# Kernel optimization log

Hardware: AMD Instinct MI355X
Metric: run time of the kernel (lower is better)

Reference implementation:

```python
import jax, jax.numpy as jnp
import numpy as np
from jax import lax

N_STEPS = 96
N_MAT = 4
N_STRIKES = 201
PERIOD = N_STEPS // N_MAT  # 24
BATCH = 8192
T_HORIZON = 2.0
RFR = 0.05
S0 = 100.0
DT = T_HORIZON / N_STEPS
SQRT_DT = DT ** 0.5
DF = float(np.exp(-RFR * DT))  # one-step discount factor


def _drift_nets(p, x):
    # x: [3, B]; three stacked MLPs (sigma_S, b_V, sigma_V), n=net axis -> [3, 1, B]
    W0, b0, W1, b1, W2, b2, W3, b3 = p
    h = jax.nn.relu(jnp.einsum('nof,fb->nob', W0, x) + b0[:, :, None])
    h = jax.nn.relu(jnp.einsum('nof,nfb->nob', W1, h) + b1[:, :, None])
    h = jax.nn.relu(jnp.einsum('nof,nfb->nob', W2, h) + b2[:, :, None])
    return jnp.einsum('nof,nfb->nob', W3, h) + b3[:, :, None]


def _hedge_net(p, x):
    # x: [2, B] -> [N_STRIKES*N_MAT, B]
    W0, b0, W1, b1, W2, b2, W3, b3, W4, b4 = p
    h = jax.nn.relu(W0 @ x + b0[:, None])
    h = jax.nn.relu(W1 @ h + b1[:, None])
    h = jax.nn.relu(W2 @ h + b2[:, None])
    h = jax.nn.relu(W3 @ h + b3[:, None])
    return W4 @ h + b4[:, None]


def _forward(nW0, nb0, nW1, nb1, nW2, nb2, nW3, nb3,
             hW0, hb0, hW1, hb1, hW2, hb2, hW3, hb3, hW4, hb4,
             rho, V0, strikes, noise1, noise2, remat=False):
    dtype = noise1.dtype
    B = noise1.shape[1]
    rho_s = rho[0]
    S = jnp.full((B,), S0, dtype)
    V = jnp.ones((B,), dtype) * V0[0]
    H = jnp.zeros((N_STRIKES, N_MAT, B), dtype)  # hedging accumulator
    prices = jnp.zeros((N_STRIKES, N_MAT), dtype)
    variance = jnp.zeros((N_STRIKES, N_MAT), dtype)
    for m in range(N_MAT):  # one MLP set per maturity period (timegridNet idx)
        nP = (nW0[:, m], nb0[:, m], nW1[:, m], nb1[:, m],
              nW2[:, m], nb2[:, m], nW3[:, m], nb3[:, m])
        hP = (hW0[m], hb0[m], hW1[m], hb1[m], hW2[m], hb2[m],
              hW3[m], hb3[m], hW4[m], hb4[m])

        def step(carry, xs, nP=nP, hP=hP):
            S, V, H = carry
            t_i, n1, n2 = xs
            t = t_i * jnp.ones_like(S)
            X = jnp.stack([t, S, V], 0)  # [3, B]
            raw = _drift_nets(nP, X)
            raw_d = _drift_nets(nP, lax.stop_gradient(X))  # X.detach() path
            vals = raw / (1.0 + jnp.abs(raw_d) * SQRT_DT)
            sig_S, b_V, sig_V = vals[0, 0], vals[1, 0], vals[2, 0]
            b_S = S * RFR / (1.0 + jnp.abs(lax.stop_gradient(S) * RFR) * SQRT_DT)
            dW = SQRT_DT * n2
            dB = rho_s * dW + jnp.sqrt(1.0 - rho_s ** 2) * SQRT_DT * n1
            S_new = S + b_S * DT + sig_S * dB
            V_new = jax.nn.relu(V + b_V * DT + sig_V * dW)  # clamp(.., 0)
            hedge = _hedge_net(hP, jnp.stack([t, lax.stop_gradient(S)], 0))
            hedge = hedge.reshape(N_STRIKES, N_MAT, -1)
            H_new = H + DF * lax.stop_gradient(S) * lax.stop_gradient(sig_S) * hedge * dW
            return (S_new, V_new, H_new), None

        if remat:
            step = jax.checkpoint(step)
        ts = (jnp.arange(PERIOD, dtype=dtype) + m * PERIOD) * DT  # (i-1)*dt
        xs = (ts, noise1[m * PERIOD:(m + 1) * PERIOD], noise2[m * PERIOD:(m + 1) * PERIOD])
        (S, V, H), _ = lax.scan(step, (S, V, H), xs)
        disc = DF ** ((m + 1) * PERIOD)
        payoff = disc * jax.nn.relu(S[None, :] - strikes) - H[:, m]  # [201, B]
        prices = prices.at[:, m].set(jnp.mean(payoff, axis=1))
        variance = variance.at[:, m].set(jnp.var(payoff, axis=1, ddof=1))  # torch unbiased var
    return prices, variance


def setup_inputs() -> dict:
    key = jax.random.key(0)
    ks = jax.random.split(key, 24)
    f32 = jnp.float32

    def w(k, shape, fan_in):
        return (jax.random.normal(k, shape, f32) / np.sqrt(fan_in)).astype(f32)

    def b(k, shape):
        return 0.01 * jax.random.normal(k, shape, f32)

    inp = {}
    inp['nW0'] = w(ks[0], (3, 4, 32, 3), 3)
    inp['nb0'] = b(ks[1], (3, 4, 32))
    inp['nW1'] = w(ks[2], (3, 4, 32, 32), 32)
    inp['nb1'] = b(ks[3], (3, 4, 32))
    inp['nW2'] = w(ks[4], (3, 4, 32, 32), 32)
    inp['nb2'] = b(ks[5], (3, 4, 32))
    inp['nW3'] = w(ks[6], (3, 4, 1, 32), 32)
    inp['nb3'] = b(ks[7], (3, 4, 1))
    inp['hW0'] = w(ks[8], (4, 64, 2), 2)
    inp['hb0'] = b(ks[9], (4, 64))
    inp['hW1'] = w(ks[10], (4, 64, 64), 64)
    inp['hb1'] = b(ks[11], (4, 64))
    inp['hW2'] = w(ks[12], (4, 64, 64), 64)
    inp['hb2'] = b(ks[13], (4, 64))
    inp['hW3'] = w(ks[14], (4, 64, 64), 64)
    inp['hb3'] = b(ks[15], (4, 64))
    inp['hW4'] = w(ks[16], (4, 804, 64), 64)
    inp['hb4'] = b(ks[17], (4, 804))
    inp['rho'] = jnp.array([0.3], f32)
    inp['V0'] = jnp.array([0.04], f32)
    inp['strikes'] = jnp.linspace(50.0, 150.0, N_STRIKES, dtype=f32).reshape(-1, 1)
    inp['noise1'] = jax.random.normal(ks[18], (N_STEPS, BATCH), f32)
    inp['noise2'] = jax.random.normal(ks[19], (N_STEPS, BATCH), f32)
    return inp


def reference(nW0, nb0, nW1, nb1, nW2, nb2, nW3, nb3,
              hW0, hb0, hW1, hb1, hW2, hb2, hW3, hb3, hW4, hb4,
              rho, V0, strikes, noise1, noise2):
    return _forward(nW0, nb0, nW1, nb1, nW2, nb2, nW3, nb3,
                    hW0, hb0, hW1, hb1, hW2, hb2, hW3, hb3, hW4, hb4,
                    rho, V0, strikes, noise1, noise2)
```

## Files before the change

### kernel.cpp

```cpp
#include <hip/hip_runtime.h>
#include <math.h>

#define TPB      128
#define NBLOCKS  512
#define PPB      16
#define BATCHN   8192
#define NMAT     4
#define PERS     24
#define NK       201
#define DSTR     124
#define HSTR     76
#define GSTR     68
#define GSC      (1.0f/4096.0f)
#define GUNSC    4096.0f

typedef _Float16 f16;
typedef _Float16 f16x4 __attribute__((ext_vector_type(4)));
typedef _Float16 f16x8 __attribute__((ext_vector_type(8)));
typedef float    f32x4 __attribute__((ext_vector_type(4)));

template<int N> struct IC { static constexpr int v = N; };

#define LDS_FENCE() asm volatile("s_waitcnt lgkmcnt(0)" ::: "memory")

__device__ __forceinline__ f16x8 relu8(f16x8 v){
#pragma unroll
  for (int i = 0; i < 8; ++i) v[i] = (v[i] > (f16)0.f) ? v[i] : (f16)0.f;
  return v;
}
__device__ __forceinline__ f16x8 cvt88(float4 a, float4 b){
  f16x8 r;
  r[0]=(f16)a.x; r[1]=(f16)a.y; r[2]=(f16)a.z; r[3]=(f16)a.w;
  r[4]=(f16)b.x; r[5]=(f16)b.y; r[6]=(f16)b.z; r[7]=(f16)b.w;
  return r;
}
__device__ __forceinline__ f16x4 cvt4(float4 a){
  f16x4 r; r[0]=(f16)a.x; r[1]=(f16)a.y; r[2]=(f16)a.z; r[3]=(f16)a.w; return r;
}

__global__ __launch_bounds__(TPB, 1)
void sde_kernel(const float* __restrict__ nW0, const float* __restrict__ nb0,
                const float* __restrict__ nW1, const float* __restrict__ nb1,
                const float* __restrict__ nW2, const float* __restrict__ nb2,
                const float* __restrict__ nW3, const float* __restrict__ nb3,
                const float* __restrict__ hW0, const float* __restrict__ hb0,
                const float* __restrict__ hW1, const float* __restrict__ hb1,
                const float* __restrict__ hW2, const float* __restrict__ hb2,
                const float* __restrict__ hW3, const float* __restrict__ hb3,
                const float* __restrict__ hW4, const float* __restrict__ hb4,
                const float* __restrict__ rho, const float* __restrict__ V0,
                const float* __restrict__ strikes,
                const float* __restrict__ noise1, const float* __restrict__ noise2,
                float* __restrict__ part1, float* __restrict__ part2)
{
  __shared__ __align__(16) f16   bbD [PPB*DSTR];
  __shared__ __align__(16) f16   bbH1[PPB*HSTR];
  __shared__ __align__(16) f16   bbH2[PPB*HSTR];
  __shared__ __align__(16) float Gsave[NMAT*PPB*GSTR];
  __shared__ float mbS[2][PPB], mbc[2][PPB];
  __shared__ float CstL[NMAT*PPB];
  __shared__ float SfinL[PPB];
  __shared__ float strikesL[NK];

  const int tid  = threadIdx.x;
  const int wv   = tid >> 6;
  const int lane = tid & 63;
  const int L15  = lane & 15;
  const int G    = lane >> 4;
  const int gpath = blockIdx.x * PPB + L15;

  const float DTf = (float)(2.0/96.0);
  const float SDT = 0.14433756729740643f;
  const float DFf = (float)exp(-0.05 * 2.0 / 96.0);
  const float rho_s = rho[0];
  const float rt1m  = sqrtf(1.f - rho_s*rho_s);

  for (int k = tid; k < NK; k += TPB) strikesL[k] = strikes[k];

  float S = 100.f, Vv = V0[0];
  __syncthreads();

  auto maturity = [&](auto MC){
    constexpr int m = decltype(MC)::v;

    f16x8 aD1[6], aD2[6];  f16x4 bD1r[6], bD2r[6];  f32x4 w3r[6];
    f16x8 w0r[3][4];       float b30=0.f, b31=0.f, b32=0.f;
    f16x8 aH[3][4][2];     f16x4 bHr[3][4];         f16x8 wh0r[2][3];
    float Gacc[16];        float Cacc = 0.f;
    float pn1 = 0.f, pn2 = 0.f;

    if (wv == 0){
#pragma unroll
      for (int t6 = 0; t6 < 6; ++t6){
        const int n  = t6 >> 1;
        const int o  = ((t6 & 1) << 4) + L15;
        const int ob = ((t6 & 1) << 4) + 4*G;
        const float* p1 = nW1 + (size_t)(((n*4+m)*32)+o)*32 + G*8;
        aD1[t6] = cvt88(*(const float4*)p1, *(const float4*)(p1+4));
        const float* p2 = nW2 + (size_t)(((n*4+m)*32)+o)*32 + G*8;
        aD2[t6] = cvt88(*(const float4*)p2, *(const float4*)(p2+4));
        bD1r[t6] = cvt4(*(const float4*)(nb1 + (n*4+m)*32 + ob));
        bD2r[t6] = cvt4(*(const float4*)(nb2 + (n*4+m)*32 + ob));
        w3r[t6]  = *(const f32x4*)(nW3 + (n*4+m)*32 + ob);
      }
      b30 = nb3[m]; b31 = nb3[4+m]; b32 = nb3[8+m];
#pragma unroll
      for (int n = 0; n < 3; ++n){
        f16x8 wt, ws, wvv, bz;
#pragma unroll
        for (int j = 0; j < 8; ++j){
          const int o = G*8 + j;
          const float* p = nW0 + (size_t)(((n*4+m)*32)+o)*3;
          wt[j]=(f16)p[0]; ws[j]=(f16)p[1]; wvv[j]=(f16)p[2];
          bz[j]=(f16)nb0[(n*4+m)*32+o];
        }
        w0r[n][0]=wt; w0r[n][1]=ws; w0r[n][2]=wvv; w0r[n][3]=bz;
      }
      pn1 = noise1[(size_t)(m*PERS)*BATCHN + gpath];
      pn2 = noise2[(size_t)(m*PERS)*BATCHN + gpath];
    } else {
#pragma unroll
      for (int L = 0; L < 3; ++L){
        const float* W = (L==0)?hW1:(L==1)?hW2:hW3;
        const float* B = (L==0)?hb1:(L==1)?hb2:hb3;
#pragma unroll
        for (int mt = 0; mt < 4; ++mt){
#pragma unroll
          for (int kt = 0; kt < 2; ++kt){
            const float* src = W + (size_t)m*4096 + (16*mt + L15)*64 + kt*32 + G*8;
            aH[L][mt][kt] = cvt88(*(const float4*)src, *(const float4*)(src+4));
          }
          bHr[L][mt] = cvt4(*(const float4*)(B + m*64 + mt*16 + 4*G));
        }
      }
#pragma unroll
      for (int kt = 0; kt < 2; ++kt){
        f16x8 wt, ws, bz;
#pragma unroll
        for (int j = 0; j < 8; ++j){
          const int o = kt*32 + G*8 + j;
          wt[j]=(f16)hW0[m*128 + o*2];
          ws[j]=(f16)hW0[m*128 + o*2 + 1];
          bz[j]=(f16)hb0[m*64 + o];
        }
        wh0r[kt][0]=wt; wh0r[kt][1]=ws; wh0r[kt][2]=bz;
      }
#pragma unroll
      for (int j = 0; j < 16; ++j) Gacc[j] = 0.f;
    }

#pragma unroll 1
    for (int i = 0; i <= PERS; ++i){
      if (wv == 0){
        if (i < PERS){
          const int gstep = m*PERS + i;
          const float t = (float)gstep * DTf;
          if (lane < PPB) mbS[i & 1][L15] = S;
          float nn1 = 0.f, nn2 = 0.f;
          if (i+1 < PERS){
            nn1 = noise1[(size_t)(gstep+1)*BATCHN + gpath];
            nn2 = noise2[(size_t)(gstep+1)*BATCHN + gpath];
          }
          const f16 th=(f16)t, Sh=(f16)S, Vh=(f16)Vv;
          f16x8 bfr[3];
#pragma unroll
          for (int n = 0; n < 3; ++n)
            bfr[n] = relu8(w0r[n][0]*th + w0r[n][1]*Sh + w0r[n][2]*Vh + w0r[n][3]);
#pragma unroll
          for (int t6 = 0; t6 < 6; ++t6){
            f32x4 acc = {(float)bD1r[t6][0],(float)bD1r[t6][1],(float)bD1r[t6][2],(float)bD1r[t6][3]};
            acc = __builtin_amdgcn_mfma_f32_16x16x32_f16(aD1[t6], bfr[t6>>1], acc, 0,0,0);
            f16x4 o4;
            o4[0]=(f16)fmaxf(acc[0],0.f); o4[1]=(f16)fmaxf(acc[1],0.f);
            o4[2]=(f16)fmaxf(acc[2],0.f); o4[3]=(f16)fmaxf(acc[3],0.f);
            *(f16x4*)&bbD[L15*DSTR + t6*16 + 4*G] = o4;
          }
          LDS_FENCE();
          f16x8 bl[3];
#pragma unroll
          for (int n = 0; n < 3; ++n)
            bl[n] = *(const f16x8*)&bbD[L15*DSTR + n*32 + G*8];
          f32x4 c2[6];
#pragma unroll
          for (int t6 = 0; t6 < 6; ++t6){
            f32x4 acc = {(float)bD2r[t6][0],(float)bD2r[t6][1],(float)bD2r[t6][2],(float)bD2r[t6][3]};
            c2[t6] = __builtin_amdgcn_mfma_f32_16x16x32_f16(aD2[t6], bl[t6>>1], acc, 0,0,0);
          }
          float pr0=0.f, pr1=0.f, pr2=0.f;
#pragma unroll
          for (int t6 = 0; t6 < 6; ++t6){
            const f32x4 w4 = w3r[t6];
            const float pp = w4[0]*fmaxf(c2[t6][0],0.f)+w4[1]*fmaxf(c2[t6][1],0.f)
                           + w4[2]*fmaxf(c2[t6][2],0.f)+w4[3]*fmaxf(c2[t6][3],0.f);
            if (t6<2) pr0+=pp; else if (t6<4) pr1+=pp; else pr2+=pp;
          }
          pr0 += __shfl_xor(pr0,16); pr0 += __shfl_xor(pr0,32);
          pr1 += __shfl_xor(pr1,16); pr1 += __shfl_xor(pr1,32);
          pr2 += __shfl_xor(pr2,16); pr2 += __shfl_xor(pr2,32);
          const float r0=pr0+b30, r1=pr1+b31, r2=pr2+b32;
          const float sigS = r0/(1.f+fabsf(r0)*SDT);
          const float bV   = r1/(1.f+fabsf(r1)*SDT);
          const float sigV = r2/(1.f+fabsf(r2)*SDT);
          const float sr = S*0.05f;
          const float bS = sr/(1.f+fabsf(sr)*SDT);
          const float dW = SDT*pn2;
          const float dB = rho_s*dW + rt1m*SDT*pn1;
          const float c  = DFf*S*sigS*dW;
          Cacc += c;
          if (lane < PPB) mbc[i & 1][L15] = c;
          S  = S + bS*DTf + sigS*dB;
          Vv = fmaxf(Vv + bV*DTf + sigV*dW, 0.f);
          pn1 = nn1; pn2 = nn2;
        }
      } else {
        if (i >= 1){
          const int s = i - 1;
          const float t = (float)(m*PERS + s) * DTf;
          const float Sj = mbS[s & 1][L15];
          const float c  = mbc[s & 1][L15];
          const f16 th=(f16)t, Sh=(f16)Sj;
          f16x8 bh0 = relu8(wh0r[0][0]*th + wh0r[0][1]*Sh + wh0r[0][2]);
          f16x8 bh1 = relu8(wh0r[1][0]*th + wh0r[1][1]*Sh + wh0r[1][2]);
#pragma unroll
          for (int mt = 0; mt < 4; ++mt){
            f32x4 acc = {(float)bHr[0][mt][0],(float)bHr[0][mt][1],(float)bHr[0][mt][2],(float)bHr[0][mt][3]};
            acc = __builtin_amdgcn_mfma_f32_16x16x32_f16(aH[0][mt][0], bh0, acc, 0,0,0);
            acc = __builtin_amdgcn_mfma_f32_16x16x32_f16(aH[0][mt][1], bh1, acc, 0,0,0);
            f16x4 o4;
            o4[0]=(f16)fmaxf(acc[0],0.f); o4[1]=(f16)fmaxf(acc[1],0.f);
            o4[2]=(f16)fmaxf(acc[2],0.f); o4[3]=(f16)fmaxf(acc[3],0.f);
            *(f16x4*)&bbH1[L15*HSTR + mt*16 + 4*G] = o4;
          }
          LDS_FENCE();
          f16x8 x0 = *(const f16x8*)&bbH1[L15*HSTR +      G*8];
          f16x8 x1 = *(const f16x8*)&bbH1[L15*HSTR + 32 + G*8];
#pragma unroll
          for (int mt = 0; mt < 4; ++mt){
            f32x4 acc = {(float)bHr[1][mt][0],(float)bHr[1][mt][1],(float)bHr[1][mt][2],(float)bHr[1][mt][3]};
            acc = __builtin_amdgcn_mfma_f32_16x16x32_f16(aH[1][mt][0], x0, acc, 0,0,0);
            acc = __builtin_amdgcn_mfma_f32_16x16x32_f16(aH[1][mt][1], x1, acc, 0,0,0);
            f16x4 o4;
            o4[0]=(f16)fmaxf(acc[0],0.f); o4[1]=(f16)fmaxf(acc[1],0.f);
            o4[2]=(f16)fmaxf(acc[2],0.f); o4[3]=(f16)fmaxf(acc[3],0.f);
            *(f16x4*)&bbH2[L15*HSTR + mt*16 + 4*G] = o4;
          }
          LDS_FENCE();
          x0 = *(const f16x8*)&bbH2[L15*HSTR +      G*8];
          x1 = *(const f16x8*)&bbH2[L15*HSTR + 32 + G*8];
#pragma unroll
          for (int mt = 0; mt < 4; ++mt){
            f32x4 acc = {(float)bHr[2][mt][0],(float)bHr[2][mt][1],(float)bHr[2][mt][2],(float)bHr[2][mt][3]};
            acc = __builtin_amdgcn_mfma_f32_16x16x32_f16(aH[2][mt][0], x0, acc, 0,0,0);
            acc = __builtin_amdgcn_mfma_f32_16x16x32_f16(aH[2][mt][1], x1, acc, 0,0,0);
            Gacc[mt*4+0] += c*fmaxf(acc[0],0.f);
            Gacc[mt*4+1] += c*fmaxf(acc[1],0.f);
            Gacc[mt*4+2] += c*fmaxf(acc[2],0.f);
            Gacc[mt*4+3] += c*fmaxf(acc[3],0.f);
          }
        }
      }
      __syncthreads();
    }

    if (wv == 0){
      if (lane < PPB){ SfinL[L15] = S; CstL[m*PPB + L15] = Cacc; }
    } else {
#pragma unroll
      for (int mt = 0; mt < 4; ++mt){
        f32x4 gv = {Gacc[mt*4+0], Gacc[mt*4+1], Gacc[mt*4+2], Gacc[mt*4+3]};
        *(f32x4*)&Gsave[(size_t)(m*PPB + L15)*GSTR + mt*16 + 4*G] = gv;
      }
    }
    __syncthreads();

    {
      const float discm = (float)exp(-0.05*(2.0/96.0)*(double)(PERS*(m+1)));
      const float Sfin = SfinL[L15];
      float Cc[m+1];
      f16x8 Bf[m+1][2];
#pragma unroll
      for (int q = 0; q <= m; ++q){
        Cc[q] = CstL[q*PPB + L15];
#pragma unroll
        for (int kt = 0; kt < 2; ++kt){
          const float* gp = &Gsave[(size_t)(q*PPB + L15)*GSTR + kt*32 + G*8];
          const f32x4 g0 = *(const f32x4*)gp;
          const f32x4 g1 = *(const f32x4*)(gp + 4);
          f16x8 b;
          b[0]=(f16)(g0[0]*GSC); b[1]=(f16)(g0[1]*GSC); b[2]=(f16)(g0[2]*GSC); b[3]=(f16)(g0[3]*GSC);
          b[4]=(f16)(g1[0]*GSC); b[5]=(f16)(g1[1]*GSC); b[6]=(f16)(g1[2]*GSC); b[7]=(f16)(g1[3]*GSC);
          Bf[q][kt] = b;
        }
      }
      for (int mt = wv; mt < 13; mt += 2){
        const int ksr = min(16*mt + L15, 200);
        f32x4 acc = {0.f, 0.f, 0.f, 0.f};
#pragma unroll
        for (int q = 0; q <= m; ++q){
#pragma unroll
          for (int kt = 0; kt < 2; ++kt){
            const float* ap = hW4 + (size_t)(q*804 + ksr*4 + m)*64 + kt*32 + G*8;
            const f16x8 a = cvt88(*(const float4*)ap, *(const float4*)(ap+4));
            acc = __builtin_amdgcn_mfma_f32_16x16x32_f16(a, Bf[q][kt], acc, 0,0,0);
          }
        }
#pragma unroll
        for (int r = 0; r < 4; ++r){
          const int k2  = 16*mt + 4*G + r;
          const int k2c = min(k2, 200);
          float ac = acc[r] * GUNSC;
#pragma unroll
          for (int q = 0; q <= m; ++q)
            ac = fmaf(hb4[q*804 + k2c*4 + m], Cc[q], ac);
          const float pay = discm*fmaxf(Sfin - strikesL[k2c], 0.f) - ac;
          float s1 = pay, s2 = pay*pay;
          s1 += __shfl_xor(s1,1); s1 += __shfl_xor(s1,2);
          s1 += __shfl_xor(s1,4); s1 += __shfl_xor(s1,8);
          s2 += __shfl_xor(s2,1); s2 += __shfl_xor(s2,2);
          s2 += __shfl_xor(s2,4); s2 += __shfl_xor(s2,8);
          if (L15 == 0 && k2 < NK){
            part1[(size_t)(m*NK + k2)*NBLOCKS + blockIdx.x] = s1;
            part2[(size_t)(m*NK + k2)*NBLOCKS + blockIdx.x] = s2;
          }
        }
      }
    }
  };

  maturity(IC<0>{});
  maturity(IC<1>{});
  maturity(IC<2>{});
  maturity(IC<3>{});
}

__global__ __launch_bounds__(256)
void finalize_kernel(const float* __restrict__ part1,
                     const float* __restrict__ part2,
                     float* __restrict__ out)
{
  const int j   = blockIdx.x;
  const int m   = j / NK, k = j % NK;
  const int tid = threadIdx.x;
  double s1 = (double)part1[(size_t)j*NBLOCKS + tid]
            + (double)part1[(size_t)j*NBLOCKS + 256 + tid];
  double s2 = (double)part2[(size_t)j*NBLOCKS + tid]
            + (double)part2[(size_t)j*NBLOCKS + 256 + tid];
#pragma unroll
  for (int d = 32; d > 0; d >>= 1){
    s1 += __shfl_down(s1, d, 64);
    s2 += __shfl_down(s2, d, 64);
  }
  __shared__ double r1[4], r2[4];
  if ((tid & 63) == 0){ r1[tid>>6] = s1; r2[tid>>6] = s2; }
  __syncthreads();
  if (tid == 0){
    const double t1 = r1[0]+r1[1]+r1[2]+r1[3];
    const double t2 = r2[0]+r2[1]+r2[2]+r2[3];
    const double mean = t1 / 8192.0;
    const double var  = (t2 - t1*t1/8192.0) / 8191.0;
    out[k*NMAT + m]            = (float)mean;
    out[NK*NMAT + k*NMAT + m]  = (float)var;
  }
}

extern "C" void kernel_launch(void* const* d_in, const int* in_sizes, int n_in,
                              void* d_out, int out_size, void* d_ws, size_t ws_size,
                              hipStream_t stream)
{
  (void)in_sizes; (void)n_in; (void)out_size; (void)ws_size;
  const float* nW0 = (const float*)d_in[0];
  const float* nb0 = (const float*)d_in[1];
  const float* nW1 = (const float*)d_in[2];
  const float* nb1 = (const float*)d_in[3];
  const float* nW2 = (const float*)d_in[4];
  const float* nb2 = (const float*)d_in[5];
  const float* nW3 = (const float*)d_in[6];
  const float* nb3 = (const float*)d_in[7];
  const float* hW0 = (const float*)d_in[8];
  const float* hb0 = (const float*)d_in[9];
  const float* hW1 = (const float*)d_in[10];
  const float* hb1 = (const float*)d_in[11];
  const float* hW2 = (const float*)d_in[12];
  const float* hb2 = (const float*)d_in[13];
  const float* hW3 = (const float*)d_in[14];
  const float* hb3 = (const float*)d_in[15];
  const float* hW4 = (const float*)d_in[16];
  const float* hb4 = (const float*)d_in[17];
  const float* rho = (const float*)d_in[18];
  const float* V0  = (const float*)d_in[19];
  const float* strikes = (const float*)d_in[20];
  const float* noise1  = (const float*)d_in[21];
  const float* noise2  = (const float*)d_in[22];

  float* part1 = (float*)d_ws;
  float* part2 = part1 + (size_t)NMAT*NK*NBLOCKS;

  sde_kernel<<<NBLOCKS, TPB, 0, stream>>>(nW0, nb0, nW1, nb1, nW2, nb2, nW3, nb3,
                                          hW0, hb0, hW1, hb1, hW2, hb2, hW3, hb3,
                                          hW4, hb4, rho, V0, strikes, noise1, noise2,
                                          part1, part2);

  finalize_kernel<<<NMAT*NK, 256, 0, stream>>>(part1, part2, (float*)d_out);
}
```

Measured before the change: 309.6 us.

## Pipeline SDE producer and hedge consumer across maturities with per-period barriers

Replaces the per-step lockstep between the drift wave and the hedge wave, which used a __syncthreads every time step, with a maturity-level software pipeline. Wave 0 simulates a whole period into double-buffered LDS arrays while wave 1 runs the hedge MLP on the previous period, two steps at a time so MFMA chains interleave. The output projection for each maturity is now done by wave 1 alone, and divisions become reciprocal approximations. This cuts barrier count from about 25 per maturity to one per phase, but the final hW4 projection loses its two-wave split and is serialized on one wave.

```diff
diff --git a/kernel.cpp b/kernel.cpp
--- a/kernel.cpp
+++ b/kernel.cpp
@@ -3,14 +3,13 @@
 
 #define TPB      128
 #define NBLOCKS  512
-#define PPB      16
 #define BATCHN   8192
 #define NMAT     4
 #define PERS     24
 #define NK       201
+#define NPG      512
 #define DSTR     124
 #define HSTR     76
-#define GSTR     68
 #define GSC      (1.0f/4096.0f)
 #define GUNSC    4096.0f
 
@@ -18,8 +17,6 @@
 typedef _Float16 f16x4 __attribute__((ext_vector_type(4)));
 typedef _Float16 f16x8 __attribute__((ext_vector_type(8)));
 typedef float    f32x4 __attribute__((ext_vector_type(4)));
-
-template<int N> struct IC { static constexpr int v = N; };
 
 #define LDS_FENCE() asm volatile("s_waitcnt lgkmcnt(0)" ::: "memory")
 
@@ -36,6 +33,9 @@
 }
 __device__ __forceinline__ f16x4 cvt4(float4 a){
   f16x4 r; r[0]=(f16)a.x; r[1]=(f16)a.y; r[2]=(f16)a.z; r[3]=(f16)a.w; return r;
+}
+__device__ __forceinline__ float sdiv(float x, float s){
+  return x * __builtin_amdgcn_rcpf(fmaf(fabsf(x), s, 1.f));
 }
 
 __global__ __launch_bounds__(TPB, 1)
@@ -53,21 +53,18 @@
                 const float* __restrict__ noise1, const float* __restrict__ noise2,
                 float* __restrict__ part1, float* __restrict__ part2)
 {
-  __shared__ __align__(16) f16   bbD [PPB*DSTR];
-  __shared__ __align__(16) f16   bbH1[PPB*HSTR];
-  __shared__ __align__(16) f16   bbH2[PPB*HSTR];
-  __shared__ __align__(16) float Gsave[NMAT*PPB*GSTR];
-  __shared__ float mbS[2][PPB], mbc[2][PPB];
-  __shared__ float CstL[NMAT*PPB];
-  __shared__ float SfinL[PPB];
-  __shared__ float strikesL[NK];
+  __shared__ __align__(16) f16   bbD[16*DSTR];
+  __shared__ __align__(16) f16   bbH[4][16*HSTR];
+  __shared__ float SP[2][PERS][16], CP[2][PERS][16];
+  __shared__ float SfinAll[NMAT][16], CstAll[NMAT][16];
+  __shared__ float Gsave[NMAT][64][17];
 
   const int tid  = threadIdx.x;
   const int wv   = tid >> 6;
   const int lane = tid & 63;
   const int L15  = lane & 15;
   const int G    = lane >> 4;
-  const int gpath = blockIdx.x * PPB + L15;
+  const int gpath = blockIdx.x * 16 + L15;
 
   const float DTf = (float)(2.0/96.0);
   const float SDT = 0.14433756729740643f;
@@ -75,262 +72,253 @@
   const float rho_s = rho[0];
   const float rt1m  = sqrtf(1.f - rho_s*rho_s);
 
-  for (int k = tid; k < NK; k += TPB) strikesL[k] = strikes[k];
-
   float S = 100.f, Vv = V0[0];
-  __syncthreads();
-
-  auto maturity = [&](auto MC){
-    constexpr int m = decltype(MC)::v;
-
-    f16x8 aD1[6], aD2[6];  f16x4 bD1r[6], bD2r[6];  f32x4 w3r[6];
-    f16x8 w0r[3][4];       float b30=0.f, b31=0.f, b32=0.f;
-    f16x8 aH[3][4][2];     f16x4 bHr[3][4];         f16x8 wh0r[2][3];
-    float Gacc[16];        float Cacc = 0.f;
-    float pn1 = 0.f, pn2 = 0.f;
-
-    if (wv == 0){
+
+  auto produce = [&](int m){
+    f16x8 aD1[6], aD2[6];  f32x4 bD1r[6], bD2r[6], w3r[6];
+    f16x8 w0r[3][4];
+#pragma unroll
+    for (int t6 = 0; t6 < 6; ++t6){
+      const int n  = t6 >> 1;
+      const int o  = ((t6 & 1) << 4) + L15;
+      const int ob = ((t6 & 1) << 4) + 4*G;
+      const float* p1 = nW1 + (size_t)(((n*4+m)*32)+o)*32 + G*8;
+      aD1[t6] = cvt88(*(const float4*)p1, *(const float4*)(p1+4));
+      const float* p2 = nW2 + (size_t)(((n*4+m)*32)+o)*32 + G*8;
+      aD2[t6] = cvt88(*(const float4*)p2, *(const float4*)(p2+4));
+      bD1r[t6] = *(const f32x4*)(nb1 + (n*4+m)*32 + ob);
+      bD2r[t6] = *(const f32x4*)(nb2 + (n*4+m)*32 + ob);
+      w3r[t6]  = *(const f32x4*)(nW3 + (n*4+m)*32 + ob);
+    }
+    const float b30 = nb3[m], b31 = nb3[4+m], b32 = nb3[8+m];
+#pragma unroll
+    for (int n = 0; n < 3; ++n){
+      f16x8 wt, ws, wvv, bz;
+#pragma unroll
+      for (int j = 0; j < 8; ++j){
+        const int o = G*8 + j;
+        const float* p = nW0 + (size_t)(((n*4+m)*32)+o)*3;
+        wt[j]=(f16)p[0]; ws[j]=(f16)p[1]; wvv[j]=(f16)p[2];
+        bz[j]=(f16)nb0[(n*4+m)*32+o];
+      }
+      w0r[n][0]=wt; w0r[n][1]=ws; w0r[n][2]=wvv; w0r[n][3]=bz;
+    }
+    float pn1 = noise1[(size_t)(m*PERS)*BATCHN + gpath];
+    float pn2 = noise2[(size_t)(m*PERS)*BATCHN + gpath];
+    float Cacc = 0.f;
+    const int b = m & 1;
+
+#pragma unroll 1
+    for (int s = 0; s < PERS; ++s){
+      const int gstep = m*PERS + s;
+      const float t = (float)gstep * DTf;
+      float nn1 = 0.f, nn2 = 0.f;
+      if (s+1 < PERS){
+        nn1 = noise1[(size_t)(gstep+1)*BATCHN + gpath];
+        nn2 = noise2[(size_t)(gstep+1)*BATCHN + gpath];
+      }
+      const f16 th=(f16)t, Sh=(f16)S, Vh=(f16)Vv;
+      f16x8 bfr[3];
+#pragma unroll
+      for (int n = 0; n < 3; ++n)
+        bfr[n] = relu8(w0r[n][0]*th + w0r[n][1]*Sh + w0r[n][2]*Vh + w0r[n][3]);
 #pragma unroll
       for (int t6 = 0; t6 < 6; ++t6){
-        const int n  = t6 >> 1;
-        const int o  = ((t6 & 1) << 4) + L15;
-        const int ob = ((t6 & 1) << 4) + 4*G;
-        const float* p1 = nW1 + (size_t)(((n*4+m)*32)+o)*32 + G*8;
-        aD1[t6] = cvt88(*(const float4*)p1, *(const float4*)(p1+4));
-        const float* p2 = nW2 + (size_t)(((n*4+m)*32)+o)*32 + G*8;
-        aD2[t6] = cvt88(*(const float4*)p2, *(const float4*)(p2+4));
-        bD1r[t6] = cvt4(*(const float4*)(nb1 + (n*4+m)*32 + ob));
-        bD2r[t6] = cvt4(*(const float4*)(nb2 + (n*4+m)*32 + ob));
-        w3r[t6]  = *(const f32x4*)(nW3 + (n*4+m)*32 + ob);
-      }
-      b30 = nb3[m]; b31 = nb3[4+m]; b32 = nb3[8+m];
-#pragma unroll
-      for (int n = 0; n < 3; ++n){
-        f16x8 wt, ws, wvv, bz;
+        f32x4 acc = {bD1r[t6][0], bD1r[t6][1], bD1r[t6][2], bD1r[t6][3]};
+        acc = __builtin_amdgcn_mfma_f32_16x16x32_f16(aD1[t6], bfr[t6>>1], acc, 0,0,0);
+        f16x4 o4;
+        o4[0]=(f16)fmaxf(acc[0],0.f); o4[1]=(f16)fmaxf(acc[1],0.f);
+        o4[2]=(f16)fmaxf(acc[2],0.f); o4[3]=(f16)fmaxf(acc[3],0.f);
+        *(f16x4*)&bbD[L15*DSTR + t6*16 + 4*G] = o4;
+      }
+      LDS_FENCE();
+      f16x8 bl[3];
+#pragma unroll
+      for (int n = 0; n < 3; ++n)
+        bl[n] = *(const f16x8*)&bbD[L15*DSTR + n*32 + G*8];
+      f32x4 c2[6];
+#pragma unroll
+      for (int t6 = 0; t6 < 6; ++t6){
+        f32x4 acc = {bD2r[t6][0], bD2r[t6][1], bD2r[t6][2], bD2r[t6][3]};
+        c2[t6] = __builtin_amdgcn_mfma_f32_16x16x32_f16(aD2[t6], bl[t6>>1], acc, 0,0,0);
+      }
+      float pr0=0.f, pr1=0.f, pr2=0.f;
+#pragma unroll
+      for (int t6 = 0; t6 < 6; ++t6){
+        const f32x4 w4 = w3r[t6];
+        const float pp = w4[0]*fmaxf(c2[t6][0],0.f)+w4[1]*fmaxf(c2[t6][1],0.f)
+                       + w4[2]*fmaxf(c2[t6][2],0.f)+w4[3]*fmaxf(c2[t6][3],0.f);
+        if (t6<2) pr0+=pp; else if (t6<4) pr1+=pp; else pr2+=pp;
+      }
+      pr0 += __shfl_xor(pr0,16); pr0 += __shfl_xor(pr0,32);
+      pr1 += __shfl_xor(pr1,16); pr1 += __shfl_xor(pr1,32);
+      pr2 += __shfl_xor(pr2,16); pr2 += __shfl_xor(pr2,32);
+      const float sigS = sdiv(pr0 + b30, SDT);
+      const float bV   = sdiv(pr1 + b31, SDT);
+      const float sigV = sdiv(pr2 + b32, SDT);
+      const float bS   = sdiv(S*0.05f, SDT);
+      const float dW = SDT*pn2;
+      const float dB = rho_s*dW + rt1m*SDT*pn1;
+      const float c  = DFf*S*sigS*dW;
+      Cacc += c;
+      if (G == 0){ SP[b][s][L15] = S; CP[b][s][L15] = c; }
+      S  = S + bS*DTf + sigS*dB;
+      Vv = fmaxf(Vv + bV*DTf + sigV*dW, 0.f);
+      pn1 = nn1; pn2 = nn2;
+    }
+    if (G == 0){ CstAll[m][L15] = Cacc; SfinAll[m][L15] = S; }
+  };
+
+  auto consume = [&](int m){
+    f16x8 aH[3][4][2];  f16x4 bHr[3][4];  f16x8 wh0r[2][3];
+#pragma unroll
+    for (int L = 0; L < 3; ++L){
+      const float* W = (L==0)?hW1:(L==1)?hW2:hW3;
+      const float* B = (L==0)?hb1:(L==1)?hb2:hb3;
+#pragma unroll
+      for (int mt = 0; mt < 4; ++mt){
+#pragma unroll
+        for (int kt = 0; kt < 2; ++kt){
+          const float* src = W + (size_t)m*4096 + (16*mt + L15)*64 + kt*32 + G*8;
+          aH[L][mt][kt] = cvt88(*(const float4*)src, *(const float4*)(src+4));
+        }
+        bHr[L][mt] = cvt4(*(const float4*)(B + m*64 + mt*16 + 4*G));
+      }
+    }
+#pragma unroll
+    for (int kt = 0; kt < 2; ++kt){
+      f16x8 wt, ws, bz;
+#pragma unroll
+      for (int j = 0; j < 8; ++j){
+        const int o = kt*32 + G*8 + j;
+        wt[j]=(f16)hW0[m*128 + o*2];
+        ws[j]=(f16)hW0[m*128 + o*2 + 1];
+        bz[j]=(f16)hb0[m*64 + o];
+      }
+      wh0r[kt][0]=wt; wh0r[kt][1]=ws; wh0r[kt][2]=bz;
+    }
+    float Gacc[16];
+#pragma unroll
+    for (int j = 0; j < 16; ++j) Gacc[j] = 0.f;
+    const int b = m & 1;
+
+#pragma unroll 1
+    for (int s = 0; s < PERS; s += 2){
+      const float t0 = (float)(m*PERS + s    ) * DTf;
+      const float t1 = (float)(m*PERS + s + 1) * DTf;
+      const float S0 = SP[b][s][L15],   c0 = CP[b][s][L15];
+      const float S1 = SP[b][s+1][L15], c1 = CP[b][s+1][L15];
+      const f16 th0=(f16)t0, Sh0=(f16)S0, th1=(f16)t1, Sh1=(f16)S1;
+      f16x8 ba0 = relu8(wh0r[0][0]*th0 + wh0r[0][1]*Sh0 + wh0r[0][2]);
+      f16x8 ba1 = relu8(wh0r[1][0]*th0 + wh0r[1][1]*Sh0 + wh0r[1][2]);
+      f16x8 bb0 = relu8(wh0r[0][0]*th1 + wh0r[0][1]*Sh1 + wh0r[0][2]);
+      f16x8 bb1 = relu8(wh0r[1][0]*th1 + wh0r[1][1]*Sh1 + wh0r[1][2]);
+#pragma unroll
+      for (int mt = 0; mt < 4; ++mt){
+        f32x4 aa = {(float)bHr[0][mt][0],(float)bHr[0][mt][1],(float)bHr[0][mt][2],(float)bHr[0][mt][3]};
+        f32x4 ab = aa;
+        aa = __builtin_amdgcn_mfma_f32_16x16x32_f16(aH[0][mt][0], ba0, aa, 0,0,0);
+        aa = __builtin_amdgcn_mfma_f32_16x16x32_f16(aH[0][mt][1], ba1, aa, 0,0,0);
+        ab = __builtin_amdgcn_mfma_f32_16x16x32_f16(aH[0][mt][0], bb0, ab, 0,0,0);
+        ab = __builtin_amdgcn_mfma_f32_16x16x32_f16(aH[0][mt][1], bb1, ab, 0,0,0);
+        f16x4 oa, ob;
+#pragma unroll
+        for (int r = 0; r < 4; ++r){ oa[r]=(f16)fmaxf(aa[r],0.f); ob[r]=(f16)fmaxf(ab[r],0.f); }
+        *(f16x4*)&bbH[0][L15*HSTR + mt*16 + 4*G] = oa;
+        *(f16x4*)&bbH[2][L15*HSTR + mt*16 + 4*G] = ob;
+      }
+      LDS_FENCE();
+      f16x8 xa0 = *(const f16x8*)&bbH[0][L15*HSTR +      G*8];
+      f16x8 xa1 = *(const f16x8*)&bbH[0][L15*HSTR + 32 + G*8];
+      f16x8 xb0 = *(const f16x8*)&bbH[2][L15*HSTR +      G*8];
+      f16x8 xb1 = *(const f16x8*)&bbH[2][L15*HSTR + 32 + G*8];
+#pragma unroll
+      for (int mt = 0; mt < 4; ++mt){
+        f32x4 aa = {(float)bHr[1][mt][0],(float)bHr[1][mt][1],(float)bHr[1][mt][2],(float)bHr[1][mt][3]};
+        f32x4 ab = aa;
+        aa = __builtin_amdgcn_mfma_f32_16x16x32_f16(aH[1][mt][0], xa0, aa, 0,0,0);
+        aa = __builtin_amdgcn_mfma_f32_16x16x32_f16(aH[1][mt][1], xa1, aa, 0,0,0);
+        ab = __builtin_amdgcn_mfma_f32_16x16x32_f16(aH[1][mt][0], xb0, ab, 0,0,0);
+        ab = __builtin_amdgcn_mfma_f32_16x16x32_f16(aH[1][mt][1], xb1, ab, 0,0,0);
+        f16x4 oa, ob;
+#pragma unroll
+        for (int r = 0; r < 4; ++r){ oa[r]=(f16)fmaxf(aa[r],0.f); ob[r]=(f16)fmaxf(ab[r],0.f); }
+        *(f16x4*)&bbH[1][L15*HSTR + mt*16 + 4*G] = oa;
+        *(f16x4*)&bbH[3][L15*HSTR + mt*16 + 4*G] = ob;
+      }
+      LDS_FENCE();
+      xa0 = *(const f16x8*)&bbH[1][L15*HSTR +      G*8];
+      xa1 = *(const f16x8*)&bbH[1][L15*HSTR + 32 + G*8];
+      xb0 = *(const f16x8*)&bbH[3][L15*HSTR +      G*8];
+      xb1 = *(const f16x8*)&bbH[3][L15*HSTR + 32 + G*8];
+#pragma unroll
+      for (int mt = 0; mt < 4; ++mt){
+        f32x4 aa = {(float)bHr[2][mt][0],(float)bHr[2][mt][1],(float)bHr[2][mt][2],(float)bHr[2][mt][3]};
+        f32x4 ab = aa;
+        aa = __builtin_amdgcn_mfma_f32_16x16x32_f16(aH[2][mt][0], xa0, aa, 0,0,0);
+        aa = __builtin_amdgcn_mfma_f32_16x16x32_f16(aH[2][mt][1], xa1, aa, 0,0,0);
+        ab = __builtin_amdgcn_mfma_f32_16x16x32_f16(aH[2][mt][0], xb0, ab, 0,0,0);
+        ab = __builtin_amdgcn_mfma_f32_16x16x32_f16(aH[2][mt][1], xb1, ab, 0,0,0);
+#pragma unroll
+        for (int r = 0; r < 4; ++r)
+          Gacc[mt*4+r] += c0*fmaxf(aa[r],0.f) + c1*fmaxf(ab[r],0.f);
+      }
+    }
+
+#pragma unroll
+    for (int mt = 0; mt < 4; ++mt)
+#pragma unroll
+      for (int r = 0; r < 4; ++r)
+        Gsave[m][mt*16 + 4*G + r][L15] = Gacc[mt*4+r];
+    LDS_FENCE();
+
+    const float discm = (float)exp(-0.05*(2.0/96.0)*(double)(PERS*(m+1)));
+    const float Sfin  = SfinAll[m][L15];
+#pragma unroll 1
+    for (int mt = 0; mt < 13; ++mt){
+      const int ksr = min(16*mt + L15, 200);
+      f32x4 acc = {0.f, 0.f, 0.f, 0.f};
+#pragma unroll 1
+      for (int q = 0; q <= m; ++q){
+        f16x8 Bq0, Bq1;
 #pragma unroll
         for (int j = 0; j < 8; ++j){
-          const int o = G*8 + j;
-          const float* p = nW0 + (size_t)(((n*4+m)*32)+o)*3;
-          wt[j]=(f16)p[0]; ws[j]=(f16)p[1]; wvv[j]=(f16)p[2];
-          bz[j]=(f16)nb0[(n*4+m)*32+o];
+          Bq0[j] = (f16)(Gsave[q][     G*8 + j][L15] * GSC);
+          Bq1[j] = (f16)(Gsave[q][32 + G*8 + j][L15] * GSC);
         }
-        w0r[n][0]=wt; w0r[n][1]=ws; w0r[n][2]=wvv; w0r[n][3]=bz;
-      }
-      pn1 = noise1[(size_t)(m*PERS)*BATCHN + gpath];
-      pn2 = noise2[(size_t)(m*PERS)*BATCHN + gpath];
-    } else {
-#pragma unroll
-      for (int L = 0; L < 3; ++L){
-        const float* W = (L==0)?hW1:(L==1)?hW2:hW3;
-        const float* B = (L==0)?hb1:(L==1)?hb2:hb3;
-#pragma unroll
-        for (int mt = 0; mt < 4; ++mt){
-#pragma unroll
-          for (int kt = 0; kt < 2; ++kt){
-            const float* src = W + (size_t)m*4096 + (16*mt + L15)*64 + kt*32 + G*8;
-            aH[L][mt][kt] = cvt88(*(const float4*)src, *(const float4*)(src+4));
-          }
-          bHr[L][mt] = cvt4(*(const float4*)(B + m*64 + mt*16 + 4*G));
+        const float* ap0 = hW4 + (size_t)(q*804 + ksr*4 + m)*64 +      G*8;
+        const float* ap1 = hW4 + (size_t)(q*804 + ksr*4 + m)*64 + 32 + G*8;
+        acc = __builtin_amdgcn_mfma_f32_16x16x32_f16(cvt88(*(const float4*)ap0, *(const float4*)(ap0+4)), Bq0, acc, 0,0,0);
+        acc = __builtin_amdgcn_mfma_f32_16x16x32_f16(cvt88(*(const float4*)ap1, *(const float4*)(ap1+4)), Bq1, acc, 0,0,0);
+      }
+#pragma unroll
+      for (int r = 0; r < 4; ++r){
+        const int k2  = 16*mt + 4*G + r;
+        const int k2c = min(k2, 200);
+        float ac = acc[r] * GUNSC;
+#pragma unroll 1
+        for (int q = 0; q <= m; ++q)
+          ac = fmaf(hb4[q*804 + k2c*4 + m], CstAll[q][L15], ac);
+        const float pay = discm*fmaxf(Sfin - strikes[k2c], 0.f) - ac;
+        float s1 = pay, s2 = pay*pay;
+        s1 += __shfl_xor(s1,1); s1 += __shfl_xor(s1,2);
+        s1 += __shfl_xor(s1,4); s1 += __shfl_xor(s1,8);
+        s2 += __shfl_xor(s2,1); s2 += __shfl_xor(s2,2);
+        s2 += __shfl_xor(s2,4); s2 += __shfl_xor(s2,8);
+        if (L15 == 0 && k2 < NK){
+          part1[(size_t)(m*NK + k2)*NPG + blockIdx.x] = s1;
+          part2[(size_t)(m*NK + k2)*NPG + blockIdx.x] = s2;
         }
       }
-#pragma unroll
-      for (int kt = 0; kt < 2; ++kt){
-        f16x8 wt, ws, bz;
-#pragma unroll
-        for (int j = 0; j < 8; ++j){
-          const int o = kt*32 + G*8 + j;
-          wt[j]=(f16)hW0[m*128 + o*2];
-          ws[j]=(f16)hW0[m*128 + o*2 + 1];
-          bz[j]=(f16)hb0[m*64 + o];
-        }
-        wh0r[kt][0]=wt; wh0r[kt][1]=ws; wh0r[kt][2]=bz;
-      }
-#pragma unroll
-      for (int j = 0; j < 16; ++j) Gacc[j] = 0.f;
-    }
-
-#pragma unroll 1
-    for (int i = 0; i <= PERS; ++i){
-      if (wv == 0){
-        if (i < PERS){
-          const int gstep = m*PERS + i;
-          const float t = (float)gstep * DTf;
-          if (lane < PPB) mbS[i & 1][L15] = S;
-          float nn1 = 0.f, nn2 = 0.f;
-          if (i+1 < PERS){
-            nn1 = noise1[(size_t)(gstep+1)*BATCHN + gpath];
-            nn2 = noise2[(size_t)(gstep+1)*BATCHN + gpath];
-          }
-          const f16 th=(f16)t, Sh=(f16)S, Vh=(f16)Vv;
-          f16x8 bfr[3];
-#pragma unroll
-          for (int n = 0; n < 3; ++n)
-            bfr[n] = relu8(w0r[n][0]*th + w0r[n][1]*Sh + w0r[n][2]*Vh + w0r[n][3]);
-#pragma unroll
-          for (int t6 = 0; t6 < 6; ++t6){
-            f32x4 acc = {(float)bD1r[t6][0],(float)bD1r[t6][1],(float)bD1r[t6][2],(float)bD1r[t6][3]};
-            acc = __builtin_amdgcn_mfma_f32_16x16x32_f16(aD1[t6], bfr[t6>>1], acc, 0,0,0);
-            f16x4 o4;
-            o4[0]=(f16)fmaxf(acc[0],0.f); o4[1]=(f16)fmaxf(acc[1],0.f);
-            o4[2]=(f16)fmaxf(acc[2],0.f); o4[3]=(f16)fmaxf(acc[3],0.f);
-            *(f16x4*)&bbD[L15*DSTR + t6*16 + 4*G] = o4;
-          }
-          LDS_FENCE();
-          f16x8 bl[3];
-#pragma unroll
-          for (int n = 0; n < 3; ++n)
-            bl[n] = *(const f16x8*)&bbD[L15*DSTR + n*32 + G*8];
-          f32x4 c2[6];
-#pragma unroll
-          for (int t6 = 0; t6 < 6; ++t6){
-            f32x4 acc = {(float)bD2r[t6][0],(float)bD2r[t6][1],(float)bD2r[t6][2],(float)bD2r[t6][3]};
-            c2[t6] = __builtin_amdgcn_mfma_f32_16x16x32_f16(aD2[t6], bl[t6>>1], acc, 0,0,0);
-          }
-          float pr0=0.f, pr1=0.f, pr2=0.f;
-#pragma unroll
-          for (int t6 = 0; t6 < 6; ++t6){
-            const f32x4 w4 = w3r[t6];
-            const float pp = w4[0]*fmaxf(c2[t6][0],0.f)+w4[1]*fmaxf(c2[t6][1],0.f)
-                           + w4[2]*fmaxf(c2[t6][2],0.f)+w4[3]*fmaxf(c2[t6][3],0.f);
-            if (t6<2) pr0+=pp; else if (t6<4) pr1+=pp; else pr2+=pp;
-          }
-          pr0 += __shfl_xor(pr0,16); pr0 += __shfl_xor(pr0,32);
-          pr1 += __shfl_xor(pr1,16); pr1 += __shfl_xor(pr1,32);
-          pr2 += __shfl_xor(pr2,16); pr2 += __shfl_xor(pr2,32);
-          const float r0=pr0+b30, r1=pr1+b31, r2=pr2+b32;
-          const float sigS = r0/(1.f+fabsf(r0)*SDT);
-          const float bV   = r1/(1.f+fabsf(r1)*SDT);
-          const float sigV = r2/(1.f+fabsf(r2)*SDT);
-          const float sr = S*0.05f;
-          const float bS = sr/(1.f+fabsf(sr)*SDT);
-          const float dW = SDT*pn2;
-          const float dB = rho_s*dW + rt1m*SDT*pn1;
-          const float c  = DFf*S*sigS*dW;
-          Cacc += c;
-          if (lane < PPB) mbc[i & 1][L15] = c;
-          S  = S + bS*DTf + sigS*dB;
-          Vv = fmaxf(Vv + bV*DTf + sigV*dW, 0.f);
-          pn1 = nn1; pn2 = nn2;
-        }
-      } else {
-        if (i >= 1){
-          const int s = i - 1;
-          const float t = (float)(m*PERS + s) * DTf;
-          const float Sj = mbS[s & 1][L15];
-          const float c  = mbc[s & 1][L15];
-          const f16 th=(f16)t, Sh=(f16)Sj;
-          f16x8 bh0 = relu8(wh0r[0][0]*th + wh0r[0][1]*Sh + wh0r[0][2]);
-          f16x8 bh1 = relu8(wh0r[1][0]*th + wh0r[1][1]*Sh + wh0r[1][2]);
-#pragma unroll
-          for (int mt = 0; mt < 4; ++mt){
-            f32x4 acc = {(float)bHr[0][mt][0],(float)bHr[0][mt][1],(float)bHr[0][mt][2],(float)bHr[0][mt][3]};
-            acc = __builtin_amdgcn_mfma_f32_16x16x32_f16(aH[0][mt][0], bh0, acc, 0,0,0);
-            acc = __builtin_amdgcn_mfma_f32_16x16x32_f16(aH[0][mt][1], bh1, acc, 0,0,0);
-            f16x4 o4;
-            o4[0]=(f16)fmaxf(acc[0],0.f); o4[1]=(f16)fmaxf(acc[1],0.f);
-            o4[2]=(f16)fmaxf(acc[2],0.f); o4[3]=(f16)fmaxf(acc[3],0.f);
-            *(f16x4*)&bbH1[L15*HSTR + mt*16 + 4*G] = o4;
-          }
-          LDS_FENCE();
-          f16x8 x0 = *(const f16x8*)&bbH1[L15*HSTR +      G*8];
-          f16x8 x1 = *(const f16x8*)&bbH1[L15*HSTR + 32 + G*8];
-#pragma unroll
-          for (int mt = 0; mt < 4; ++mt){
-            f32x4 acc = {(float)bHr[1][mt][0],(float)bHr[1][mt][1],(float)bHr[1][mt][2],(float)bHr[1][mt][3]};
-            acc = __builtin_amdgcn_mfma_f32_16x16x32_f16(aH[1][mt][0], x0, acc, 0,0,0);
-            acc = __builtin_amdgcn_mfma_f32_16x16x32_f16(aH[1][mt][1], x1, acc, 0,0,0);
-            f16x4 o4;
-            o4[0]=(f16)fmaxf(acc[0],0.f); o4[1]=(f16)fmaxf(acc[1],0.f);
-            o4[2]=(f16)fmaxf(acc[2],0.f); o4[3]=(f16)fmaxf(acc[3],0.f);
-            *(f16x4*)&bbH2[L15*HSTR + mt*16 + 4*G] = o4;
-          }
-          LDS_FENCE();
-          x0 = *(const f16x8*)&bbH2[L15*HSTR +      G*8];
-          x1 = *(const f16x8*)&bbH2[L15*HSTR + 32 + G*8];
-#pragma unroll
-          for (int mt = 0; mt < 4; ++mt){
-            f32x4 acc = {(float)bHr[2][mt][0],(float)bHr[2][mt][1],(float)bHr[2][mt][2],(float)bHr[2][mt][3]};
-            acc = __builtin_amdgcn_mfma_f32_16x16x32_f16(aH[2][mt][0], x0, acc, 0,0,0);
-            acc = __builtin_amdgcn_mfma_f32_16x16x32_f16(aH[2][mt][1], x1, acc, 0,0,0);
-            Gacc[mt*4+0] += c*fmaxf(acc[0],0.f);
-            Gacc[mt*4+1] += c*fmaxf(acc[1],0.f);
-            Gacc[mt*4+2] += c*fmaxf(acc[2],0.f);
-            Gacc[mt*4+3] += c*fmaxf(acc[3],0.f);
-          }
-        }
-      }
-      __syncthreads();
-    }
-
-    if (wv == 0){
-      if (lane < PPB){ SfinL[L15] = S; CstL[m*PPB + L15] = Cacc; }
-    } else {
-#pragma unroll
-      for (int mt = 0; mt < 4; ++mt){
-        f32x4 gv = {Gacc[mt*4+0], Gacc[mt*4+1], Gacc[mt*4+2], Gacc[mt*4+3]};
-        *(f32x4*)&Gsave[(size_t)(m*PPB + L15)*GSTR + mt*16 + 4*G] = gv;
-      }
-    }
+    }
+  };
+
+#pragma unroll 1
+  for (int ph = 0; ph < 5; ++ph){
+    if (wv == 0 && ph < 4)  produce(ph);
+    if (wv == 1 && ph >= 1) consume(ph - 1);
     __syncthreads();
-
-    {
-      const float discm = (float)exp(-0.05*(2.0/96.0)*(double)(PERS*(m+1)));
-      const float Sfin = SfinL[L15];
-      float Cc[m+1];
-      f16x8 Bf[m+1][2];
-#pragma unroll
-      for (int q = 0; q <= m; ++q){
-        Cc[q] = CstL[q*PPB + L15];
-#pragma unroll
-        for (int kt = 0; kt < 2; ++kt){
-          const float* gp = &Gsave[(size_t)(q*PPB + L15)*GSTR + kt*32 + G*8];
-          const f32x4 g0 = *(const f32x4*)gp;
-          const f32x4 g1 = *(const f32x4*)(gp + 4);
-          f16x8 b;
-          b[0]=(f16)(g0[0]*GSC); b[1]=(f16)(g0[1]*GSC); b[2]=(f16)(g0[2]*GSC); b[3]=(f16)(g0[3]*GSC);
-          b[4]=(f16)(g1[0]*GSC); b[5]=(f16)(g1[1]*GSC); b[6]=(f16)(g1[2]*GSC); b[7]=(f16)(g1[3]*GSC);
-          Bf[q][kt] = b;
-        }
-      }
-      for (int mt = wv; mt < 13; mt += 2){
-        const int ksr = min(16*mt + L15, 200);
-        f32x4 acc = {0.f, 0.f, 0.f, 0.f};
-#pragma unroll
-        for (int q = 0; q <= m; ++q){
-#pragma unroll
-          for (int kt = 0; kt < 2; ++kt){
-            const float* ap = hW4 + (size_t)(q*804 + ksr*4 + m)*64 + kt*32 + G*8;
-            const f16x8 a = cvt88(*(const float4*)ap, *(const float4*)(ap+4));
-            acc = __builtin_amdgcn_mfma_f32_16x16x32_f16(a, Bf[q][kt], acc, 0,0,0);
-          }
-        }
-#pragma unroll
-        for (int r = 0; r < 4; ++r){
-          const int k2  = 16*mt + 4*G + r;
-          const int k2c = min(k2, 200);
-          float ac = acc[r] * GUNSC;
-#pragma unroll
-          for (int q = 0; q <= m; ++q)
-            ac = fmaf(hb4[q*804 + k2c*4 + m], Cc[q], ac);
-          const float pay = discm*fmaxf(Sfin - strikesL[k2c], 0.f) - ac;
-          float s1 = pay, s2 = pay*pay;
-          s1 += __shfl_xor(s1,1); s1 += __shfl_xor(s1,2);
-          s1 += __shfl_xor(s1,4); s1 += __shfl_xor(s1,8);
-          s2 += __shfl_xor(s2,1); s2 += __shfl_xor(s2,2);
-          s2 += __shfl_xor(s2,4); s2 += __shfl_xor(s2,8);
-          if (L15 == 0 && k2 < NK){
-            part1[(size_t)(m*NK + k2)*NBLOCKS + blockIdx.x] = s1;
-            part2[(size_t)(m*NK + k2)*NBLOCKS + blockIdx.x] = s2;
-          }
-        }
-      }
-    }
-  };
-
-  maturity(IC<0>{});
-  maturity(IC<1>{});
-  maturity(IC<2>{});
-  maturity(IC<3>{});
+  }
 }
 
 __global__ __launch_bounds__(256)
@@ -341,10 +329,10 @@
   const int j   = blockIdx.x;
   const int m   = j / NK, k = j % NK;
   const int tid = threadIdx.x;
-  double s1 = (double)part1[(size_t)j*NBLOCKS + tid]
-            + (double)part1[(size_t)j*NBLOCKS + 256 + tid];
-  double s2 = (double)part2[(size_t)j*NBLOCKS + tid]
-            + (double)part2[(size_t)j*NBLOCKS + 256 + tid];
+  double s1 = (double)part1[(size_t)j*NPG + tid]
+            + (double)part1[(size_t)j*NPG + 256 + tid];
+  double s2 = (double)part2[(size_t)j*NPG + tid]
+            + (double)part2[(size_t)j*NPG + 256 + tid];
 #pragma unroll
   for (int d = 32; d > 0; d >>= 1){
     s1 += __shfl_down(s1, d, 64);
@@ -393,7 +381,7 @@
   const float* noise2  = (const float*)d_in[22];
 
   float* part1 = (float*)d_ws;
-  float* part2 = part1 + (size_t)NMAT*NK*NBLOCKS;
+  float* part2 = part1 + (size_t)NMAT*NK*NPG;
 
   sde_kernel<<<NBLOCKS, TPB, 0, stream>>>(nW0, nb0, nW1, nb1, nW2, nb2, nW3, nb3,
                                           hW0, hb0, hW1, hb1, hW2, hb2, hW3, hb3,
```

Result: slower. 399.0 us (+28.9%).
